# Optimization experiments

Measured on AMD Instinct MI355X. Metric: run time of the kernel, lower is better.

Reference implementation:

```python
import jax, jax.numpy as jnp
import numpy as np


def _apply_rope(x, cos, sin):
    # x: [B, h, T, d]; cos/sin: [T, d//2]
    B, h, T, d = x.shape
    xp = x.astype(jnp.float32).reshape(B, h, T, d // 2, 2)
    xr, xi = xp[..., 0], xp[..., 1]
    c = cos[None, None]  # [1,1,T,d//2]
    s = sin[None, None]
    out_r = xr * c - xi * s
    out_i = xr * s + xi * c
    out = jnp.stack([out_r, out_i], axis=-1).reshape(B, h, T, d)
    return out.astype(x.dtype)


def setup_inputs() -> dict:
    key = jax.random.key(0)
    ks = jax.random.split(key, 7)
    B, T, C = 1, 4096, 1024
    h = 16
    d = C // h
    return {
        "x": jax.random.normal(ks[0], (B, T, C), jnp.float32),
        "freqs_cos": jax.random.normal(ks[1], (T, d // 2), jnp.float32),
        "freqs_sin": jax.random.normal(ks[2], (T, d // 2), jnp.float32),
        "Wq": jax.random.normal(ks[3], (C, C), jnp.float32) * 0.02,
        "Wk": jax.random.normal(ks[4], (C, C), jnp.float32) * 0.02,
        "Wv": jax.random.normal(ks[5], (C, C), jnp.float32) * 0.02,
        "Wo": jax.random.normal(ks[6], (C, C), jnp.float32) * 0.02,
    }


def reference(x, freqs_cos, freqs_sin, Wq, Wk, Wv, Wo):
    B, T, C = x.shape
    h = 16
    d = C // h
    # nn.Linear(bias=False): y = x @ W^T, W is [out, in]
    q = jnp.einsum("btc,oc->bto", x, Wq).reshape(B, T, h, d).transpose(0, 2, 1, 3)
    k = jnp.einsum("btc,oc->bto", x, Wk).reshape(B, T, h, d).transpose(0, 2, 1, 3)
    v = jnp.einsum("btc,oc->bto", x, Wv).reshape(B, T, h, d).transpose(0, 2, 1, 3)
    q = _apply_rope(q, freqs_cos, freqs_sin)
    k = _apply_rope(k, freqs_cos, freqs_sin)
    scale = 1.0 / jnp.sqrt(jnp.asarray(d, x.dtype))
    scores = jnp.einsum("bhqd,bhkd->bhqk", q, k) * scale  # [B,h,T,T]
    causal = jnp.tril(jnp.ones((T, T), bool))
    scores = jnp.where(causal[None, None], scores, -jnp.inf)
    att = jax.nn.softmax(scores.astype(jnp.float32), axis=-1).astype(q.dtype)
    y = jnp.einsum("bhqk,bhkd->bhqd", att, v)
    y = y.transpose(0, 2, 1, 3).reshape(B, T, C)
    return jnp.einsum("btc,oc->bto", y, Wo)  # dropout p=0 (eval)
```

## Files before the change

kernel.cpp:

```cpp
#include <hip/hip_runtime.h>
#include <hip/hip_bf16.h>
#include <math.h>

#define TT 4096
#define CC 1024
#define NH 16
#define HD 64

typedef unsigned short ushortT;
typedef __attribute__((ext_vector_type(8))) short short8;
typedef __attribute__((ext_vector_type(4))) float f32x4;

#define GLOAD_LDS16(gp, lp)                                                   \
    __builtin_amdgcn_global_load_lds(                                         \
        (const __attribute__((address_space(1))) void*)(gp),                  \
        (__attribute__((address_space(3))) void*)(lp), 16, 0, 0)

#define EXP2F(x) __builtin_amdgcn_exp2f(x)

__device__ __forceinline__ ushortT f2bf(float f) {
    __hip_bfloat16 h = __float2bfloat16(f);
    ushortT u; __builtin_memcpy(&u, &h, 2); return u;
}

#define PSLOT_BYTES 16896
#define QB_SPLIT 40
#define NCHUNK 88

__global__ __launch_bounds__(256) void cvt_all(
    const float* __restrict__ x,  const float* __restrict__ wq,
    const float* __restrict__ wk, const float* __restrict__ wv,
    const float* __restrict__ wo,
    ushortT* __restrict__ xb,  ushortT* __restrict__ wqb,
    ushortT* __restrict__ wkb, ushortT* __restrict__ wvb,
    ushortT* __restrict__ wob)
{
    const int i = (blockIdx.x * 256 + threadIdx.x) * 4;
    const int NX = TT * CC, NW = CC * CC;
    const float* s; ushortT* d; int off;
    if (i < NX)               { s = x;  d = xb;  off = i; }
    else if (i < NX + NW)     { s = wq; d = wqb; off = i - NX; }
    else if (i < NX + 2 * NW) { s = wk; d = wkb; off = i - NX - NW; }
    else if (i < NX + 3 * NW) { s = wv; d = wvb; off = i - NX - 2 * NW; }
    else                      { s = wo; d = wob; off = i - NX - 3 * NW; }
    float4 v = *(const float4*)(s + off);
    *(ushort4*)(d + off) = make_ushort4(f2bf(v.x), f2bf(v.y), f2bf(v.z), f2bf(v.w));
}

__global__ __launch_bounds__(256) void gemm_qkv(
    const ushortT* __restrict__ A,
    const ushortT* __restrict__ Bq, const ushortT* __restrict__ Bk,
    const ushortT* __restrict__ Bv,
    const float* __restrict__ fcos, const float* __restrict__ fsin,
    ushortT* __restrict__ q16, ushortT* __restrict__ k16,
    ushortT* __restrict__ vt16)
{
    __shared__ char lds[49152];

    const int z = blockIdx.z;
    const ushortT* B = (z == 0) ? Bq : (z == 1) ? Bk : Bv;

    const int lin = (int)(blockIdx.y * gridDim.x + blockIdx.x);
    const int nwg8 = (int)((gridDim.x * gridDim.y) >> 3);
    const int swz = (lin & 7) * nwg8 + (lin >> 3);
    const int bm = (swz % (int)gridDim.x) * 128;
    const int bn = (swz / (int)gridDim.x) * 128;
    const int tid = threadIdx.x;
    const int w = tid >> 6, l = tid & 63;
    const int wm = w >> 1, wn = w & 1;

    f32x4 acc[4][4] = {};

    auto stageg = [&](int kk, int base) {
        #pragma unroll
        for (int e = 0; e < 2; ++e) {
            const int D = (w * 2 + e) * 1024 + l * 16;
            const int r = D >> 6;
            const int c = (D & 63) >> 1;
            GLOAD_LDS16(A + (size_t)(bm + r) * CC + kk + c, lds + base + (w * 2 + e) * 1024);
            GLOAD_LDS16(B + (size_t)(bn + r) * CC + kk + c, lds + base + 8192 + (w * 2 + e) * 1024);
        }
    };

    stageg(0, 0);
    stageg(32, 16384);

    for (int kt = 0; kt < 32; ++kt) {
        const int cur = kt % 3;
        if (kt + 2 < 32) {
            stageg((kt + 2) * 32, ((kt + 2) % 3) * 16384);
            asm volatile("s_waitcnt vmcnt(8)" ::: "memory");
        } else if (kt + 1 < 32) {
            asm volatile("s_waitcnt vmcnt(4)" ::: "memory");
        } else {
            asm volatile("s_waitcnt vmcnt(0)" ::: "memory");
        }
        __builtin_amdgcn_s_barrier();
        __builtin_amdgcn_sched_barrier(0);

        const ushortT* As = (const ushortT*)(lds + cur * 16384);
        const ushortT* Bs = (const ushortT*)(lds + cur * 16384 + 8192);

        short8 af[4], bfr[4];
        #pragma unroll
        for (int i = 0; i < 4; ++i) {
            int row = wm * 64 + i * 16 + (l & 15);
            af[i] = *(const short8*)(As + row * 32 + (l >> 4) * 8);
        }
        #pragma unroll
        for (int j = 0; j < 4; ++j) {
            int row = wn * 64 + j * 16 + (l & 15);
            bfr[j] = *(const short8*)(Bs + row * 32 + (l >> 4) * 8);
        }
        #pragma unroll
        for (int i = 0; i < 4; ++i)
            #pragma unroll
            for (int j = 0; j < 4; ++j)
                acc[i][j] = __builtin_amdgcn_mfma_f32_16x16x32_bf16(af[i], bfr[j], acc[i][j], 0, 0, 0);
        __builtin_amdgcn_s_barrier();
    }

    if (z < 2) {
        const float rsc = (z == 0) ? 0.18033688011112042f : 1.0f;
        ushortT* dq = (z == 0) ? q16 : k16;
        float* cs = (float*)lds;
        float* sn = (float*)(lds + 16384);
        for (int idx = tid; idx < 128 * 32; idx += 256) {
            int rr = idx >> 5, cc2 = idx & 31;
            cs[idx] = fcos[(size_t)(bm + rr) * 32 + cc2];
            sn[idx] = fsin[(size_t)(bm + rr) * 32 + cc2];
        }
        __syncthreads();
        #pragma unroll
        for (int i = 0; i < 4; ++i)
            #pragma unroll
            for (int j = 0; j < 4; ++j)
                #pragma unroll
                for (int r = 0; r < 4; ++r) {
                    const int lt = wm * 64 + i * 16 + (l >> 4) * 4 + r;
                    const int o = bn + wn * 64 + j * 16 + (l & 15);
                    const float v = acc[i][j][r];
                    const float p = __shfl_xor(v, 1);
                    const int pp = (o & 63) >> 1;
                    const float cv = cs[lt * 32 + pp], sv = sn[lt * 32 + pp];
                    const float outv = ((o & 1) ? (p * sv + v * cv) : (v * cv - p * sv)) * rsc;
                    const int t = bm + lt, head = o >> 6, dd = o & 63;
                    dq[((size_t)head * TT + t) * HD + dd] = f2bf(outv);
                }
    } else {
        #pragma unroll
        for (int i = 0; i < 4; ++i)
            #pragma unroll
            for (int j = 0; j < 4; ++j)
                #pragma unroll
                for (int r = 0; r < 4; ++r) {
                    const int t = bm + wm * 64 + i * 16 + (l >> 4) * 4 + r;
                    const int o = bn + wn * 64 + j * 16 + (l & 15);
                    const int head = o >> 6, dd = o & 63;
                    const int k = t & 63;
                    const int slot = ((k & 15) << 2) | (k >> 4);
                    vt16[((size_t)(head * HD + dd)) * TT + (t & ~63) + slot] = f2bf(acc[i][j][r]);
                }
    }
}

__global__ __launch_bounds__(256) void gemm_out(
    const ushortT* __restrict__ A, const ushortT* __restrict__ B,
    float* __restrict__ dout)
{
    __shared__ char lds[49152];

    const int lin = (int)(blockIdx.y * gridDim.x + blockIdx.x);
    const int nwg8 = (int)((gridDim.x * gridDim.y) >> 3);
    const int swz = (lin & 7) * nwg8 + (lin >> 3);
    const int bm = (swz % (int)gridDim.x) * 128;
    const int bn = (swz / (int)gridDim.x) * 128;
    const int tid = threadIdx.x;
    const int w = tid >> 6, l = tid & 63;
    const int wm = w >> 1, wn = w & 1;

    f32x4 acc[4][4] = {};

    auto stageg = [&](int kk, int base) {
        #pragma unroll
        for (int e = 0; e < 2; ++e) {
            const int D = (w * 2 + e) * 1024 + l * 16;
            const int r = D >> 6;
            const int c = (D & 63) >> 1;
            GLOAD_LDS16(A + (size_t)(bm + r) * CC + kk + c, lds + base + (w * 2 + e) * 1024);
            GLOAD_LDS16(B + (size_t)(bn + r) * CC + kk + c, lds + base + 8192 + (w * 2 + e) * 1024);
        }
    };

    stageg(0, 0);
    stageg(32, 16384);

    for (int kt = 0; kt < 32; ++kt) {
        const int cur = kt % 3;
        if (kt + 2 < 32) {
            stageg((kt + 2) * 32, ((kt + 2) % 3) * 16384);
            asm volatile("s_waitcnt vmcnt(8)" ::: "memory");
        } else if (kt + 1 < 32) {
            asm volatile("s_waitcnt vmcnt(4)" ::: "memory");
        } else {
            asm volatile("s_waitcnt vmcnt(0)" ::: "memory");
        }
        __builtin_amdgcn_s_barrier();
        __builtin_amdgcn_sched_barrier(0);

        const ushortT* As = (const ushortT*)(lds + cur * 16384);
        const ushortT* Bs = (const ushortT*)(lds + cur * 16384 + 8192);

        short8 af[4], bfr[4];
        #pragma unroll
        for (int i = 0; i < 4; ++i) {
            int row = wm * 64 + i * 16 + (l & 15);
            af[i] = *(const short8*)(As + row * 32 + (l >> 4) * 8);
        }
        #pragma unroll
        for (int j = 0; j < 4; ++j) {
            int row = wn * 64 + j * 16 + (l & 15);
            bfr[j] = *(const short8*)(Bs + row * 32 + (l >> 4) * 8);
        }
        #pragma unroll
        for (int i = 0; i < 4; ++i)
            #pragma unroll
            for (int j = 0; j < 4; ++j)
                acc[i][j] = __builtin_amdgcn_mfma_f32_16x16x32_bf16(af[i], bfr[j], acc[i][j], 0, 0, 0);
        __builtin_amdgcn_s_barrier();
    }

    #pragma unroll
    for (int i = 0; i < 4; ++i)
        #pragma unroll
        for (int j = 0; j < 4; ++j)
            #pragma unroll
            for (int r = 0; r < 4; ++r) {
                const int t = bm + wm * 64 + i * 16 + (l >> 4) * 4 + r;
                const int o = bn + wn * 64 + j * 16 + (l & 15);
                dout[(size_t)t * CC + o] = acc[i][j][r];
            }
}

__global__ __launch_bounds__(256) void attn_mfma(
    const ushortT* __restrict__ q16, const ushortT* __restrict__ k16,
    const ushortT* __restrict__ vt16, ushortT* __restrict__ y16,
    char* __restrict__ parts, int* __restrict__ counter)
{
    const int tid = threadIdx.x;
    const int w = tid >> 6, l = tid & 63;

    __shared__ char lds[40960];
    char* Pbase = lds + 32768 + w * 2048;

    for (;;) {
        if (tid == 0) {
            int tk0 = atomicAdd(counter, 1);
            *(int*)lds = tk0;
        }
        __syncthreads();
        const int tk = *(const int*)lds;
        __syncthreads();
        if (tk >= NCHUNK * NH) break;

        const int head = tk / NCHUNK;
        const int cid = 87 - (tk - head * NCHUNK);
        int qb, ci, kb0, kb1;
        if (cid < QB_SPLIT) { qb = cid; ci = -1; kb0 = 0; kb1 = qb; }
        else {
            const int idx = cid - QB_SPLIT;
            qb = QB_SPLIT + (idx >> 1);
            ci = idx & 1;
            const int mid = (qb + 1) >> 1;
            kb0 = ci ? mid : 0;
            kb1 = ci ? qb : mid - 1;
        }

        const int qrow = qb * 64 + w * 16 + (l & 15);
        short8 qa[2];
        {
            const ushortT* qp = q16 + ((size_t)head * TT + qrow) * HD + (l >> 4) * 8;
            qa[0] = *(const short8*)(qp);
            qa[1] = *(const short8*)(qp + 32);
        }

        f32x4 yacc[4] = {};
        float m_r[4], l_r[4];
        #pragma unroll
        for (int r = 0; r < 4; ++r) { m_r[r] = -1e30f; l_r[r] = 0.0f; }

        auto stage = [&](int kb, int base) {
            #pragma unroll
            for (int e = 0; e < 2; ++e) {
                const int D = (w * 2 + e) * 1024 + l * 16;
                const int row = D >> 7;
                const int src = D ^ ((row & 7) << 4);
                const int col = (src & 127) >> 1;
                GLOAD_LDS16(k16 + ((size_t)head * TT + (size_t)kb * 64 + row) * HD + col,
                            lds + base + (w * 2 + e) * 1024);
                GLOAD_LDS16(vt16 + ((size_t)head * HD + row) * TT + (size_t)kb * 64 + col,
                            lds + base + 8192 + (w * 2 + e) * 1024);
            }
        };

        int cur = 0;
        stage(kb0, 0);

        for (int kb = kb0; kb <= kb1; ++kb) {
            if (kb + 1 <= kb1) {
                stage(kb + 1, (cur ^ 1) * 16384);
                asm volatile("s_waitcnt vmcnt(4)" ::: "memory");
            } else {
                asm volatile("s_waitcnt vmcnt(0)" ::: "memory");
            }
            __builtin_amdgcn_s_barrier();
            __builtin_amdgcn_sched_barrier(0);

            const char* Ks  = lds + cur * 16384;
            const char* Vts = Ks + 8192;

            f32x4 s[4] = {};
            #pragma unroll
            for (int ks = 0; ks < 2; ++ks)
                #pragma unroll
                for (int kg = 0; kg < 4; ++kg) {
                    const int key = kg * 16 + (l & 15);
                    int b = key * 128 + ks * 64 + (l >> 4) * 16;
                    b ^= (key & 7) << 4;
                    short8 kf = *(const short8*)(Ks + b);
                    s[kg] = __builtin_amdgcn_mfma_f32_16x16x32_bf16(qa[ks], kf, s[kg], 0, 0, 0);
                }

            if (kb == qb) {
                const int qg = qb * 64 + w * 16 + (l >> 4) * 4;
                #pragma unroll
                for (int kg = 0; kg < 4; ++kg)
                    #pragma unroll
                    for (int r = 0; r < 4; ++r)
                        if (kb * 64 + kg * 16 + (l & 15) > qg + r) s[kg][r] = -1e30f;
            }

            float ilmax[4];
            bool need = false;
            #pragma unroll
            for (int r = 0; r < 4; ++r) {
                const float m0 = fmaxf(fmaxf(s[0][r], s[1][r]), fmaxf(s[2][r], s[3][r]));
                ilmax[r] = m0;
                need = need || (m0 > m_r[r] + 8.0f);
            }
            if (__any(need)) {
                #pragma unroll
                for (int r = 0; r < 4; ++r) {
                    float m0 = ilmax[r];
                    m0 = fmaxf(m0, __shfl_xor(m0, 1));
                    m0 = fmaxf(m0, __shfl_xor(m0, 2));
                    m0 = fmaxf(m0, __shfl_xor(m0, 4));
                    m0 = fmaxf(m0, __shfl_xor(m0, 8));
                    const float mnew = fmaxf(m_r[r], m0);
                    const float al = EXP2F(m_r[r] - mnew);
                    m_r[r] = mnew;
                    l_r[r] *= al;
                    #pragma unroll
                    for (int dg = 0; dg < 4; ++dg)
                        yacc[dg][r] *= al;
                }
            }
            #pragma unroll
            for (int r = 0; r < 4; ++r) {
                float ls = 0.0f;
                #pragma unroll
                for (int kg = 0; kg < 4; ++kg) {
                    float p = EXP2F(s[kg][r] - m_r[r]);
                    s[kg][r] = p;
                    ls += p;
                }
                l_r[r] += ls;
            }

            #pragma unroll
            for (int r = 0; r < 4; ++r) {
                const int qq = (l >> 4) * 4 + r;
                unsigned lo, hi;
                asm("v_cvt_pk_bf16_f32 %0, %1, %2" : "=v"(lo) : "v"(s[0][r]), "v"(s[1][r]));
                asm("v_cvt_pk_bf16_f32 %0, %1, %2" : "=v"(hi) : "v"(s[2][r]), "v"(s[3][r]));
                int b = qq * 128 + (l & 15) * 8;
                b ^= (qq & 7) << 4;
                *(uint2*)(Pbase + b) = make_uint2(lo, hi);
            }

            #pragma unroll
            for (int ks2 = 0; ks2 < 2; ++ks2) {
                const int qq = l & 15;
                int pb = qq * 128 + ks2 * 64 + (l >> 4) * 16;
                pb ^= (qq & 7) << 4;
                short8 pa = *(const short8*)(Pbase + pb);
                #pragma unroll
                for (int dg = 0; dg < 4; ++dg) {
                    const int dd = dg * 16 + (l & 15);
                    int vb = dd * 128 + ks2 * 64 + (l >> 4) * 16;
                    vb ^= (dd & 7) << 4;
                    short8 vf = *(const short8*)(Vts + vb);
                    yacc[dg] = __builtin_amdgcn_mfma_f32_16x16x32_bf16(pa, vf, yacc[dg], 0, 0, 0);
                }
            }
            __builtin_amdgcn_s_barrier();
            cur ^= 1;
        }

        float lsum[4];
        #pragma unroll
        for (int r = 0; r < 4; ++r) {
            float t = l_r[r];
            t += __shfl_xor(t, 1);
            t += __shfl_xor(t, 2);
            t += __shfl_xor(t, 4);
            t += __shfl_xor(t, 8);
            lsum[r] = t;
        }

        if (ci < 0) {
            #pragma unroll
            for (int r = 0; r < 4; ++r) lsum[r] = 1.0f / lsum[r];
            #pragma unroll
            for (int dg = 0; dg < 4; ++dg)
                #pragma unroll
                for (int r = 0; r < 4; ++r) {
                    const int t = qb * 64 + w * 16 + (l >> 4) * 4 + r;
                    const int c = head * HD + dg * 16 + (l & 15);
                    y16[(size_t)t * CC + c] = f2bf(yacc[dg][r] * lsum[r]);
                }
        } else {
            char* pb = parts + (size_t)((head * 24 + (qb - QB_SPLIT)) * 2 + ci) * PSLOT_BYTES;
            float* yp = (float*)pb;
            float* mp = (float*)(pb + 16384);
            float* lp = mp + 64;
            #pragma unroll
            for (int dg = 0; dg < 4; ++dg)
                #pragma unroll
                for (int r = 0; r < 4; ++r) {
                    const int row = w * 16 + (l >> 4) * 4 + r;
                    const int col = dg * 16 + (l & 15);
                    yp[row * 64 + col] = yacc[dg][r];
                }
            if ((l & 15) == 0) {
                #pragma unroll
                for (int r = 0; r < 4; ++r) {
                    const int row = w * 16 + (l >> 4) * 4 + r;
                    mp[row] = m_r[r];
                    lp[row] = lsum[r];
                }
            }
        }
    }
}

__global__ __launch_bounds__(256) void attn_combine(
    const char* __restrict__ parts, ushortT* __restrict__ y16)
{
    const int qb = QB_SPLIT + blockIdx.x;
    const int head = blockIdx.y;
    const int tid = threadIdx.x;
    const int row = tid >> 2;
    const int pc = tid & 3;

    const char* p0 = parts + (size_t)((head * 24 + (qb - QB_SPLIT)) * 2) * PSLOT_BYTES;
    const char* p1 = p0 + PSLOT_BYTES;
    const float* y0 = (const float*)p0;
    const float* y1 = (const float*)p1;
    const float* m0p = (const float*)(p0 + 16384);
    const float* m1p = (const float*)(p1 + 16384);
    const float m0 = m0p[row], m1 = m1p[row];
    const float l0 = m0p[64 + row], l1 = m1p[64 + row];
    const float M = fmaxf(m0, m1);
    const float w0 = EXP2F(m0 - M), w1 = EXP2F(m1 - M);
    const float Linv = 1.0f / (l0 * w0 + l1 * w1);

    const int t = qb * 64 + row;
    #pragma unroll
    for (int j = 0; j < 16; ++j) {
        const int c = pc * 16 + j;
        const float v = (y0[row * 64 + c] * w0 + y1[row * 64 + c] * w1) * Linv;
        y16[(size_t)t * CC + head * HD + c] = f2bf(v);
    }
}

extern "C" void kernel_launch(void* const* d_in, const int* in_sizes, int n_in,
                              void* d_out, int out_size, void* d_ws, size_t ws_size,
                              hipStream_t stream) {
    const float* x    = (const float*)d_in[0];
    const float* fcos = (const float*)d_in[1];
    const float* fsin = (const float*)d_in[2];
    const float* Wq   = (const float*)d_in[3];
    const float* Wk   = (const float*)d_in[4];
    const float* Wv   = (const float*)d_in[5];
    const float* Wo   = (const float*)d_in[6];
    float* out = (float*)d_out;

    char* ws = (char*)d_ws;
    ushortT* xb  = (ushortT*)(ws);
    ushortT* wqb = (ushortT*)(ws + (8u << 20));
    ushortT* wkb = (ushortT*)(ws + (10u << 20));
    ushortT* wvb = (ushortT*)(ws + (12u << 20));
    ushortT* wob = (ushortT*)(ws + (14u << 20));
    ushortT* q16 = (ushortT*)(ws + (16u << 20));
    ushortT* k16 = (ushortT*)(ws + (24u << 20));
    ushortT* vt16 = (ushortT*)(ws + (32u << 20));
    ushortT* y16 = (ushortT*)(ws + (40u << 20));
    char* parts = ws;
    int* counter = (int*)(ws + (13u << 20));

    cvt_all<<<(TT * CC + 4 * CC * CC) / 4 / 256, 256, 0, stream>>>(
        x, Wq, Wk, Wv, Wo, xb, wqb, wkb, wvb, wob);

    dim3 qkvgrid(TT / 128, CC / 128, 3);
    gemm_qkv<<<qkvgrid, 256, 0, stream>>>(xb, wqb, wkb, wvb, fcos, fsin,
                                          q16, k16, vt16);

    hipMemsetAsync(counter, 0, 4, stream);
    attn_mfma<<<1024, 256, 0, stream>>>(q16, k16, vt16, y16, parts, counter);

    dim3 cgrid(64 - QB_SPLIT, NH);
    attn_combine<<<cgrid, 256, 0, stream>>>(parts, y16);

    dim3 ggrid(TT / 128, CC / 128);
    gemm_out<<<ggrid, 256, 0, stream>>>(y16, wob, out);
}
```

Baseline: 162.7 us.

## Compute transposed QK^T to keep P in registers and rebalance split-K attention chunks

The score MFMA now computes S^T (K as the A operand), so each lane holds probabilities for one query row across keys. The bf16-packed P can then feed the PV MFMA straight from registers, with no LDS round trip, and the V^T slot permutation is changed to match. Work splitting is rebalanced: late query blocks are cut into 3 chunks, middle ones into 2, and early ones run whole. Partial outputs are now stored in bf16 to halve partial-buffer traffic, and s_setprio is added around the MFMA sections. The risks are extra combine work for the 3-way splits and bf16 rounding error in the partial accumulators.

Result: no change. 164.9 us (+1.4%).

```diff
diff --git a/kernel.cpp b/kernel.cpp
--- a/kernel.cpp
+++ b/kernel.cpp
@@ -22,10 +22,13 @@
     __hip_bfloat16 h = __float2bfloat16(f);
     ushortT u; __builtin_memcpy(&u, &h, 2); return u;
 }
-
-#define PSLOT_BYTES 16896
-#define QB_SPLIT 40
-#define NCHUNK 88
+__device__ __forceinline__ float bf2f(ushortT u) {
+    return __uint_as_float(((unsigned)u) << 16);
+}
+
+#define PSLOT_BYTES 8704
+#define NCHUNK_H 124
+#define NTICK (NCHUNK_H * NH)
 
 __global__ __launch_bounds__(256) void cvt_all(
     const float* __restrict__ x,  const float* __restrict__ wq,
@@ -158,7 +161,8 @@
                     const int o = bn + wn * 64 + j * 16 + (l & 15);
                     const int head = o >> 6, dd = o & 63;
                     const int k = t & 63;
-                    const int slot = ((k & 15) << 2) | (k >> 4);
+                    const int slot = (k & 32) | (((k >> 2) & 3) << 3)
+                                   | (((k >> 4) & 1) << 2) | (k & 3);
                     vt16[((size_t)(head * HD + dd)) * TT + (t & ~63) + slot] = f2bf(acc[i][j][r]);
                 }
     }
@@ -249,9 +253,9 @@
 {
     const int tid = threadIdx.x;
     const int w = tid >> 6, l = tid & 63;
-
-    __shared__ char lds[40960];
-    char* Pbase = lds + 32768 + w * 2048;
+    const int g = l >> 4, q = l & 15;
+
+    __shared__ char lds[32768];
 
     for (;;) {
         if (tid == 0) {
@@ -261,33 +265,27 @@
         __syncthreads();
         const int tk = *(const int*)lds;
         __syncthreads();
-        if (tk >= NCHUNK * NH) break;
-
-        const int head = tk / NCHUNK;
-        const int cid = 87 - (tk - head * NCHUNK);
-        int qb, ci, kb0, kb1;
-        if (cid < QB_SPLIT) { qb = cid; ci = -1; kb0 = 0; kb1 = qb; }
-        else {
-            const int idx = cid - QB_SPLIT;
-            qb = QB_SPLIT + (idx >> 1);
-            ci = idx & 1;
-            const int mid = (qb + 1) >> 1;
-            kb0 = ci ? mid : 0;
-            kb1 = ci ? qb : mid - 1;
-        }
-
-        const int qrow = qb * 64 + w * 16 + (l & 15);
+        if (tk >= NTICK) break;
+
+        const int head = tk / NCHUNK_H;
+        const int t = tk - head * NCHUNK_H;
+        int qb, ci, nsplit;
+        if (t < 54)       { qb = 63 - t / 3; ci = t % 3; nsplit = 3; }
+        else if (t < 102) { int u = t - 54; qb = 45 - u / 2; ci = u % 2; nsplit = 2; }
+        else              { qb = 123 - t; ci = -1; nsplit = 1; }
+        const int kb0 = (ci < 0) ? 0 : ci * (qb + 1) / nsplit;
+        const int kb1 = (ci < 0) ? qb : (ci + 1) * (qb + 1) / nsplit - 1;
+
+        const int qrow = qb * 64 + w * 16 + q;
         short8 qa[2];
         {
-            const ushortT* qp = q16 + ((size_t)head * TT + qrow) * HD + (l >> 4) * 8;
+            const ushortT* qp = q16 + ((size_t)head * TT + qrow) * HD + g * 8;
             qa[0] = *(const short8*)(qp);
             qa[1] = *(const short8*)(qp + 32);
         }
 
         f32x4 yacc[4] = {};
-        float m_r[4], l_r[4];
-        #pragma unroll
-        for (int r = 0; r < 4; ++r) { m_r[r] = -1e30f; l_r[r] = 0.0f; }
+        float m_s = -1e30f, l_s = 0.0f;
 
         auto stage = [&](int kb, int base) {
             #pragma unroll
@@ -320,134 +318,130 @@
             const char* Vts = Ks + 8192;
 
             f32x4 s[4] = {};
+            __builtin_amdgcn_s_setprio(1);
             #pragma unroll
             for (int ks = 0; ks < 2; ++ks)
                 #pragma unroll
                 for (int kg = 0; kg < 4; ++kg) {
-                    const int key = kg * 16 + (l & 15);
-                    int b = key * 128 + ks * 64 + (l >> 4) * 16;
+                    const int key = kg * 16 + q;
+                    int b = key * 128 + ks * 64 + g * 16;
                     b ^= (key & 7) << 4;
                     short8 kf = *(const short8*)(Ks + b);
-                    s[kg] = __builtin_amdgcn_mfma_f32_16x16x32_bf16(qa[ks], kf, s[kg], 0, 0, 0);
-                }
+                    s[kg] = __builtin_amdgcn_mfma_f32_16x16x32_bf16(kf, qa[ks], s[kg], 0, 0, 0);
+                }
+            __builtin_amdgcn_s_setprio(0);
 
             if (kb == qb) {
-                const int qg = qb * 64 + w * 16 + (l >> 4) * 4;
                 #pragma unroll
                 for (int kg = 0; kg < 4; ++kg)
                     #pragma unroll
                     for (int r = 0; r < 4; ++r)
-                        if (kb * 64 + kg * 16 + (l & 15) > qg + r) s[kg][r] = -1e30f;
-            }
-
-            float ilmax[4];
-            bool need = false;
-            #pragma unroll
-            for (int r = 0; r < 4; ++r) {
-                const float m0 = fmaxf(fmaxf(s[0][r], s[1][r]), fmaxf(s[2][r], s[3][r]));
-                ilmax[r] = m0;
-                need = need || (m0 > m_r[r] + 8.0f);
-            }
-            if (__any(need)) {
-                #pragma unroll
-                for (int r = 0; r < 4; ++r) {
-                    float m0 = ilmax[r];
-                    m0 = fmaxf(m0, __shfl_xor(m0, 1));
-                    m0 = fmaxf(m0, __shfl_xor(m0, 2));
-                    m0 = fmaxf(m0, __shfl_xor(m0, 4));
-                    m0 = fmaxf(m0, __shfl_xor(m0, 8));
-                    const float mnew = fmaxf(m_r[r], m0);
-                    const float al = EXP2F(m_r[r] - mnew);
-                    m_r[r] = mnew;
-                    l_r[r] *= al;
+                        if (kb * 64 + kg * 16 + 4 * g + r > qrow) s[kg][r] = -1e30f;
+            }
+
+            float ilmax = s[0][0];
+            #pragma unroll
+            for (int kg = 0; kg < 4; ++kg)
+                #pragma unroll
+                for (int r = 0; r < 4; ++r)
+                    ilmax = fmaxf(ilmax, s[kg][r]);
+
+            if (__any(ilmax > m_s + 8.0f)) {
+                float mx = ilmax;
+                mx = fmaxf(mx, __shfl_xor(mx, 16));
+                mx = fmaxf(mx, __shfl_xor(mx, 32));
+                const float mnew = fmaxf(m_s, mx);
+                const float al = EXP2F(m_s - mnew);
+                m_s = mnew;
+                l_s *= al;
+                float aly[4];
+                #pragma unroll
+                for (int r = 0; r < 4; ++r)
+                    aly[r] = __shfl(al, 20 * g + r);
+                #pragma unroll
+                for (int dg = 0; dg < 4; ++dg)
                     #pragma unroll
-                    for (int dg = 0; dg < 4; ++dg)
-                        yacc[dg][r] *= al;
-                }
-            }
-            #pragma unroll
-            for (int r = 0; r < 4; ++r) {
-                float ls = 0.0f;
-                #pragma unroll
-                for (int kg = 0; kg < 4; ++kg) {
-                    float p = EXP2F(s[kg][r] - m_r[r]);
-                    s[kg][r] = p;
-                    ls += p;
-                }
-                l_r[r] += ls;
-            }
-
-            #pragma unroll
-            for (int r = 0; r < 4; ++r) {
-                const int qq = (l >> 4) * 4 + r;
-                unsigned lo, hi;
-                asm("v_cvt_pk_bf16_f32 %0, %1, %2" : "=v"(lo) : "v"(s[0][r]), "v"(s[1][r]));
-                asm("v_cvt_pk_bf16_f32 %0, %1, %2" : "=v"(hi) : "v"(s[2][r]), "v"(s[3][r]));
-                int b = qq * 128 + (l & 15) * 8;
-                b ^= (qq & 7) << 4;
-                *(uint2*)(Pbase + b) = make_uint2(lo, hi);
-            }
-
+                    for (int r = 0; r < 4; ++r)
+                        yacc[dg][r] *= aly[r];
+            }
+
+            unsigned U[4], V[4];
+            float ls = 0.0f;
+            #pragma unroll
+            for (int kg = 0; kg < 4; ++kg) {
+                const float p0 = EXP2F(s[kg][0] - m_s);
+                const float p1 = EXP2F(s[kg][1] - m_s);
+                const float p2 = EXP2F(s[kg][2] - m_s);
+                const float p3 = EXP2F(s[kg][3] - m_s);
+                ls += (p0 + p1) + (p2 + p3);
+                asm("v_cvt_pk_bf16_f32 %0, %1, %2" : "=v"(U[kg]) : "v"(p0), "v"(p1));
+                asm("v_cvt_pk_bf16_f32 %0, %1, %2" : "=v"(V[kg]) : "v"(p2), "v"(p3));
+            }
+            l_s += ls;
+
+            __builtin_amdgcn_s_setprio(1);
             #pragma unroll
             for (int ks2 = 0; ks2 < 2; ++ks2) {
-                const int qq = l & 15;
-                int pb = qq * 128 + ks2 * 64 + (l >> 4) * 16;
-                pb ^= (qq & 7) << 4;
-                short8 pa = *(const short8*)(Pbase + pb);
+                union { unsigned u[4]; short8 s8; } pu;
+                pu.u[0] = U[2 * ks2];     pu.u[1] = V[2 * ks2];
+                pu.u[2] = U[2 * ks2 + 1]; pu.u[3] = V[2 * ks2 + 1];
+                const short8 pa = pu.s8;
                 #pragma unroll
                 for (int dg = 0; dg < 4; ++dg) {
-                    const int dd = dg * 16 + (l & 15);
-                    int vb = dd * 128 + ks2 * 64 + (l >> 4) * 16;
+                    const int dd = dg * 16 + q;
+                    int vb = dd * 128 + ks2 * 64 + g * 16;
                     vb ^= (dd & 7) << 4;
                     short8 vf = *(const short8*)(Vts + vb);
                     yacc[dg] = __builtin_amdgcn_mfma_f32_16x16x32_bf16(pa, vf, yacc[dg], 0, 0, 0);
                 }
             }
+            __builtin_amdgcn_s_setprio(0);
             __builtin_amdgcn_s_barrier();
             cur ^= 1;
         }
 
-        float lsum[4];
-        #pragma unroll
-        for (int r = 0; r < 4; ++r) {
-            float t = l_r[r];
-            t += __shfl_xor(t, 1);
-            t += __shfl_xor(t, 2);
-            t += __shfl_xor(t, 4);
-            t += __shfl_xor(t, 8);
-            lsum[r] = t;
-        }
+        l_s += __shfl_xor(l_s, 16);
+        l_s += __shfl_xor(l_s, 32);
+        float lr[4];
+        #pragma unroll
+        for (int r = 0; r < 4; ++r)
+            lr[r] = __shfl(l_s, 20 * g + r);
 
         if (ci < 0) {
             #pragma unroll
-            for (int r = 0; r < 4; ++r) lsum[r] = 1.0f / lsum[r];
+            for (int r = 0; r < 4; ++r) lr[r] = 1.0f / lr[r];
             #pragma unroll
             for (int dg = 0; dg < 4; ++dg)
                 #pragma unroll
                 for (int r = 0; r < 4; ++r) {
-                    const int t = qb * 64 + w * 16 + (l >> 4) * 4 + r;
-                    const int c = head * HD + dg * 16 + (l & 15);
-                    y16[(size_t)t * CC + c] = f2bf(yacc[dg][r] * lsum[r]);
+                    const int trow = qb * 64 + w * 16 + 4 * g + r;
+                    const int col = head * HD + dg * 16 + q;
+                    y16[(size_t)trow * CC + col] = f2bf(yacc[dg][r] * lr[r]);
                 }
         } else {
-            char* pb = parts + (size_t)((head * 24 + (qb - QB_SPLIT)) * 2 + ci) * PSLOT_BYTES;
-            float* yp = (float*)pb;
-            float* mp = (float*)(pb + 16384);
-            float* lp = mp + 64;
+            float mr[4];
+            #pragma unroll
+            for (int r = 0; r < 4; ++r)
+                mr[r] = __shfl(m_s, 20 * g + r);
+            const int sidx = head * 102 +
+                ((qb >= 46) ? (qb - 46) * 3 + ci : 54 + (qb - 22) * 2 + ci);
+            char* pb = parts + (size_t)sidx * PSLOT_BYTES;
+            ushortT* yp = (ushortT*)pb;
+            float* mp = (float*)(pb + 8192);
+            float* lp = (float*)(pb + 8448);
             #pragma unroll
             for (int dg = 0; dg < 4; ++dg)
                 #pragma unroll
                 for (int r = 0; r < 4; ++r) {
-                    const int row = w * 16 + (l >> 4) * 4 + r;
-                    const int col = dg * 16 + (l & 15);
-                    yp[row * 64 + col] = yacc[dg][r];
-                }
-            if ((l & 15) == 0) {
+                    const int row = w * 16 + 4 * g + r;
+                    yp[row * 64 + dg * 16 + q] = f2bf(yacc[dg][r]);
+                }
+            if (q == 0) {
                 #pragma unroll
                 for (int r = 0; r < 4; ++r) {
-                    const int row = w * 16 + (l >> 4) * 4 + r;
-                    mp[row] = m_r[r];
-                    lp[row] = lsum[r];
+                    const int row = w * 16 + 4 * g + r;
+                    mp[row] = mr[r];
+                    lp[row] = lr[r];
                 }
             }
         }
@@ -457,30 +451,38 @@
 __global__ __launch_bounds__(256) void attn_combine(
     const char* __restrict__ parts, ushortT* __restrict__ y16)
 {
-    const int qb = QB_SPLIT + blockIdx.x;
+    const int qb = 22 + blockIdx.x;
     const int head = blockIdx.y;
-    const int tid = threadIdx.x;
-    const int row = tid >> 2;
-    const int pc = tid & 3;
-
-    const char* p0 = parts + (size_t)((head * 24 + (qb - QB_SPLIT)) * 2) * PSLOT_BYTES;
-    const char* p1 = p0 + PSLOT_BYTES;
-    const float* y0 = (const float*)p0;
-    const float* y1 = (const float*)p1;
-    const float* m0p = (const float*)(p0 + 16384);
-    const float* m1p = (const float*)(p1 + 16384);
-    const float m0 = m0p[row], m1 = m1p[row];
-    const float l0 = m0p[64 + row], l1 = m1p[64 + row];
-    const float M = fmaxf(m0, m1);
-    const float w0 = EXP2F(m0 - M), w1 = EXP2F(m1 - M);
-    const float Linv = 1.0f / (l0 * w0 + l1 * w1);
-
-    const int t = qb * 64 + row;
+    const int nsplit = (qb >= 46) ? 3 : 2;
+    const int base = head * 102 + ((qb >= 46) ? (qb - 46) * 3 : 54 + (qb - 22) * 2);
+    const int row = threadIdx.x >> 2;
+    const int pc = threadIdx.x & 3;
+
+    float m_i[3], l_i[3];
+    float M = -1e30f;
+    for (int i = 0; i < nsplit; ++i) {
+        const char* pb = parts + (size_t)(base + i) * PSLOT_BYTES;
+        m_i[i] = *(const float*)(pb + 8192 + row * 4);
+        l_i[i] = *(const float*)(pb + 8448 + row * 4);
+        M = fmaxf(M, m_i[i]);
+    }
+    float wgt[3], L = 0.0f;
+    for (int i = 0; i < nsplit; ++i) {
+        wgt[i] = EXP2F(m_i[i] - M);
+        L += l_i[i] * wgt[i];
+    }
+    const float Linv = 1.0f / L;
+
+    const int trow = qb * 64 + row;
     #pragma unroll
     for (int j = 0; j < 16; ++j) {
-        const int c = pc * 16 + j;
-        const float v = (y0[row * 64 + c] * w0 + y1[row * 64 + c] * w1) * Linv;
-        y16[(size_t)t * CC + head * HD + c] = f2bf(v);
+        const int col = pc * 16 + j;
+        float acc = 0.0f;
+        for (int i = 0; i < nsplit; ++i) {
+            const ushortT* yp = (const ushortT*)(parts + (size_t)(base + i) * PSLOT_BYTES);
+            acc += bf2f(yp[row * 64 + col]) * wgt[i];
+        }
+        y16[(size_t)trow * CC + head * HD + col] = f2bf(acc * Linv);
     }
 }
 
@@ -507,7 +509,7 @@
     ushortT* vt16 = (ushortT*)(ws + (32u << 20));
     ushortT* y16 = (ushortT*)(ws + (40u << 20));
     char* parts = ws;
-    int* counter = (int*)(ws + (13u << 20));
+    int* counter = (int*)(ws + (14u << 20) - 16);
 
     cvt_all<<<(TT * CC + 4 * CC * CC) / 4 / 256, 256, 0, stream>>>(
         x, Wq, Wk, Wv, Wo, xb, wqb, wkb, wvb, wob);
@@ -517,9 +519,9 @@
                                           q16, k16, vt16);
 
     hipMemsetAsync(counter, 0, 4, stream);
-    attn_mfma<<<1024, 256, 0, stream>>>(q16, k16, vt16, y16, parts, counter);
-
-    dim3 cgrid(64 - QB_SPLIT, NH);
+    attn_mfma<<<1280, 256, 0, stream>>>(q16, k16, vt16, y16, parts, counter);
+
+    dim3 cgrid(42, NH);
     attn_combine<<<cgrid, 256, 0, stream>>>(parts, y16);
 
     dim3 ggrid(TT / 128, CC / 128);
```
